# Kernel optimization log

Hardware: AMD Instinct MI355X
Metric: run time of the kernel (lower is better)

Reference implementation:

```python
import jax, jax.numpy as jnp
import numpy as np
import math

D_MODEL = 1024
NUM_HEADS = 16
D_HEAD = D_MODEL // NUM_HEADS


def setup_inputs() -> dict:
    key = jax.random.key(0)
    ks = jax.random.split(key, 15)
    B, S, D = 2, 2048, D_MODEL
    s = 1.0 / math.sqrt(D)
    inp = {
        'query': jax.random.normal(ks[0], (B, S, D), jnp.float32),
        'key': jax.random.normal(ks[1], (B, S, D), jnp.float32),
        'value': jax.random.normal(ks[2], (B, S, D), jnp.float32),
        'pos_embedding': jax.random.normal(ks[3], (B, S, D), jnp.float32),
        'Wq': jax.random.normal(ks[4], (D, D), jnp.float32) * s,
        'bq': jnp.zeros((D,), jnp.float32),
        'Wk': jax.random.normal(ks[5], (D, D), jnp.float32) * s,
        'bk': jnp.zeros((D,), jnp.float32),
        'Wv': jax.random.normal(ks[6], (D, D), jnp.float32) * s,
        'bv': jnp.zeros((D,), jnp.float32),
        'Wp': jax.random.normal(ks[7], (D, D), jnp.float32) * s,
        'bp': jnp.zeros((D,), jnp.float32),
        'Wo': jax.random.normal(ks[8], (D, D), jnp.float32) * s,
        'bo': jnp.zeros((D,), jnp.float32),
    }
    return inp


def _relative_shift(pos_score):
    # pos_score: [B, H, S1, S2] -> Transformer-XL pad/reshape/slice shift
    B, H, S1, S2 = pos_score.shape
    padded = jnp.pad(pos_score, ((0, 0), (0, 0), (0, 0), (1, 0)))  # [B,H,S1,S2+1]
    padded = padded.reshape(B, H, S2 + 1, S1)
    return padded[:, :, 1:].reshape(B, H, S1, S2)


def reference(query, key, value, pos_embedding, Wq, bq, Wk, bk, Wv, bv, Wp, bp, Wo, bo):
    B, S, D = query.shape
    H, Dh = NUM_HEADS, D_HEAD
    sqrt_dim = math.sqrt(D)

    q = (query @ Wq.T + bq).reshape(B, S, H, Dh)          # [B,S,H,Dh]
    k = (key @ Wk.T + bk).reshape(B, S, H, Dh)            # [B,S,H,Dh]
    v = (value @ Wv.T + bv).reshape(B, S, H, Dh)          # [B,S,H,Dh]
    p = (pos_embedding @ Wp.T + bp).reshape(B, S, H, Dh)  # [B,S,H,Dh]

    content_score = jnp.einsum('bqhd,bkhd->bhqk', q, k)   # [B,H,S,S]
    pos_score = jnp.einsum('bqhd,bkhd->bhqk', q, p)       # [B,H,S,S]
    pos_score = _relative_shift(pos_score)

    score = (content_score + pos_score) / sqrt_dim
    attn = jax.nn.softmax(score, axis=-1)
    context = jnp.einsum('bhqk,bkhd->bqhd', attn, v).reshape(B, S, D)
    return context @ Wo.T + bo
```

## Files before the change

### kernel.cpp

```cpp
#include <hip/hip_runtime.h>
#include <hip/hip_bf16.h>

#define S_LEN  2048
#define DMODEL 1024
#define NHEADS 16
#define DHEAD  64
#define TOKENS 4096
#define QSCALE 0.04508422f

typedef __attribute__((ext_vector_type(8))) short bf16x8;
typedef __attribute__((ext_vector_type(4))) float f32x4;

template <int M> struct IC { static constexpr int value = M; };

__device__ __forceinline__ float bf2f(unsigned short b) {
    union { unsigned u; float f; } v; v.u = ((unsigned)b) << 16;
    return v.f;
}
__device__ __forceinline__ unsigned cvt_pk_bf16(float lo, float hi) {
    unsigned r;
    asm("v_cvt_pk_bf16_f32 %0, %1, %2" : "=v"(r) : "v"(lo), "v"(hi));
    return r;
}
__device__ __forceinline__ unsigned short f2bf1(float x) {
    return (unsigned short)cvt_pk_bf16(x, x);
}
__device__ __forceinline__ void lds_fence() {
    asm volatile("s_waitcnt lgkmcnt(0)" ::: "memory");
    __builtin_amdgcn_sched_barrier(0);
}
__device__ __forceinline__ void gload_lds16(const void* g, void* l) {
    __builtin_amdgcn_global_load_lds(
        (const __attribute__((address_space(1))) void*)g,
        (__attribute__((address_space(3))) void*)l, 16, 0, 0);
}

__global__ __launch_bounds__(256) void proj_gemm(
    const float* __restrict__ x0, const float* __restrict__ x1,
    const float* __restrict__ x2, const float* __restrict__ x3,
    const float* __restrict__ w0, const float* __restrict__ w1,
    const float* __restrict__ w2, const float* __restrict__ w3,
    const float* __restrict__ b0, const float* __restrict__ b1,
    const float* __restrict__ b2, const float* __restrict__ b3,
    unsigned short* __restrict__ o0, unsigned short* __restrict__ o1,
    unsigned short* __restrict__ o2, unsigned short* __restrict__ o3)
{
    const int z = blockIdx.z;
    const float* X  = (z == 0) ? x0 : (z == 1) ? x1 : (z == 2) ? x2 : x3;
    const float* W  = (z == 0) ? w0 : (z == 1) ? w1 : (z == 2) ? w2 : w3;
    const float* Bv = (z == 0) ? b0 : (z == 1) ? b1 : (z == 2) ? b2 : b3;
    unsigned short* O = (z == 0) ? o0 : (z == 1) ? o1 : (z == 2) ? o2 : o3;

    __shared__ __align__(16) unsigned short At[128 * 40];
    __shared__ __align__(16) unsigned short Bt[128 * 40];

    const int tid  = threadIdx.x;
    const int lane = tid & 63;
    const int w    = tid >> 6;
    const int wr   = w & 1, wc = w >> 1;
    const int m0   = blockIdx.x * 128;
    const int n0   = blockIdx.y * 128;
    const int l16  = lane & 15, lq = lane >> 4;

    f32x4 acc[4][4];
    #pragma unroll
    for (int i = 0; i < 4; i++)
        #pragma unroll
        for (int j = 0; j < 4; j++) acc[i][j] = (f32x4){0.f, 0.f, 0.f, 0.f};

    for (int k0 = 0; k0 < DMODEL; k0 += 32) {
        __syncthreads();
        #pragma unroll
        for (int i = 0; i < 4; i++) {
            int e = tid + i * 256;
            int row = e >> 3, cg = e & 7;
            float4 va = *(const float4*)&X[(long)(m0 + row) * DMODEL + k0 + cg * 4];
            uint2 ua; ua.x = cvt_pk_bf16(va.x, va.y); ua.y = cvt_pk_bf16(va.z, va.w);
            *(uint2*)&At[row * 40 + cg * 4] = ua;
            float4 vb = *(const float4*)&W[(long)(n0 + row) * DMODEL + k0 + cg * 4];
            uint2 ub; ub.x = cvt_pk_bf16(vb.x, vb.y); ub.y = cvt_pk_bf16(vb.z, vb.w);
            *(uint2*)&Bt[row * 40 + cg * 4] = ub;
        }
        __syncthreads();
        bf16x8 af[4], bfr[4];
        #pragma unroll
        for (int f = 0; f < 4; f++) {
            af[f]  = *(const bf16x8*)&At[(64 * wr + 16 * f + l16) * 40 + 8 * lq];
            bfr[f] = *(const bf16x8*)&Bt[(64 * wc + 16 * f + l16) * 40 + 8 * lq];
        }
        #pragma unroll
        for (int i = 0; i < 4; i++)
            #pragma unroll
            for (int j = 0; j < 4; j++)
                acc[i][j] = __builtin_amdgcn_mfma_f32_16x16x32_bf16(af[i], bfr[j], acc[i][j], 0, 0, 0);
    }

    #pragma unroll
    for (int j = 0; j < 4; j++) {
        int n_g = n0 + 64 * wc + 16 * j + l16;
        float bias = Bv[n_g];
        int h = n_g >> 6, dh = n_g & 63;
        if (z == 2) {
            #pragma unroll
            for (int i = 0; i < 4; i++) {
                int m_g = m0 + 64 * wr + 16 * i + 4 * lq;
                int b = m_g >> 11, s = m_g & (S_LEN - 1);
                uint2 u;
                u.x = cvt_pk_bf16(acc[i][j][0] + bias, acc[i][j][1] + bias);
                u.y = cvt_pk_bf16(acc[i][j][2] + bias, acc[i][j][3] + bias);
                *(uint2*)&O[(long)(((b * NHEADS + h) * DHEAD) + dh) * S_LEN + s] = u;
            }
        } else {
            float scale = (z == 0) ? QSCALE : 1.0f;
            #pragma unroll
            for (int i = 0; i < 4; i++) {
                #pragma unroll
                for (int r = 0; r < 4; r++) {
                    int m_g = m0 + 64 * wr + 16 * i + 4 * lq + r;
                    int b = m_g >> 11, s = m_g & (S_LEN - 1);
                    O[(long)(((b * NHEADS + h) * S_LEN) + s) * DHEAD + dh] =
                        f2bf1((acc[i][j][r] + bias) * scale);
                }
            }
        }
    }
}

__global__ __launch_bounds__(256, 3) void rel_attn(
    const unsigned short* __restrict__ Q,
    const unsigned short* __restrict__ K,
    const unsigned short* __restrict__ VT,
    const unsigned short* __restrict__ P,
    unsigned short* __restrict__ CTX)
{
    __shared__ __align__(16) unsigned short Kb[64 * 64];
    __shared__ __align__(16) unsigned short P2b[128 * 64];
    __shared__ __align__(16) unsigned short WPb[4 * 1344];

    const int tid  = threadIdx.x;
    const int lane = tid & 63;
    const int w    = tid >> 6;
    const int l16  = lane & 15;
    const int lq   = lane >> 4;

    const int wg = ((blockIdx.x & 7) << 7) + (blockIdx.x >> 3);
    const int qt = wg & 31;
    const int bh = wg >> 5;
    const int q0 = qt << 6;
    const long baseQK = (long)bh * (S_LEN * DHEAD);
    const int qi_l = 16 * w + l16;

    const unsigned short* Kbh = K + baseQK;
    const unsigned short* Pbh = P + baseQK;
    const unsigned short* Vl  = VT + baseQK + (long)l16 * S_LEN + 8 * lq;

    const int gx0 = ((0 + lq) ^ (l16 & 7)) * 8;
    const int gx1 = ((4 + lq) ^ (l16 & 7)) * 8;

    bf16x8 qf0[2], qf1[2];
    {
        const unsigned short* qrow = Q + baseQK + (long)(q0 + qi_l) * DHEAD + 8 * lq;
        qf0[0] = *(const bf16x8*)(qrow);
        qf0[1] = *(const bf16x8*)(qrow + 32);
        qf1[0] = *(const bf16x8*)(qrow + DHEAD);
        qf1[1] = *(const bf16x8*)(qrow + DHEAD + 32);
    }

    const int srow = lane >> 3;
    const int sgr  = (lane & 7) ^ srow;
    auto stage_K = [&](int kr0) {
        #pragma unroll
        for (int j = 0; j < 2; ++j) {
            int idx = w * 2 + j;
            const unsigned short* src = Kbh + (long)(kr0 + idx * 8 + srow) * 64 + sgr * 8;
            gload_lds16(src, &Kb[idx * 512]);
        }
    };
    auto stage_P2 = [&](int mfirst) {
        #pragma unroll
        for (int j = 0; j < 2; ++j) {
            int idx = w * 2 + j;
            int m = mfirst + idx * 8 + srow;
            int pr = m - ((m >= 2049) ? 2049 : 0);
            const unsigned short* src = Pbh + (long)pr * 64 + sgr * 8;
            gload_lds16(src, &P2b[((mfirst + idx * 8) & 127) * 64]);
        }
    };

    float mrow = -1e30f, lrow = 0.f;
    f32x4 oacc[4];
    #pragma unroll
    for (int f = 0; f < 4; f++) oacc[f] = (f32x4){0.f, 0.f, 0.f, 0.f};

    unsigned short* tw        = &WPb[w * 1344 + l16 * 84 + 4 * lq];
    const unsigned short* tr  = &WPb[w * 1344 + l16 * 83 + 15 + 4 * lq];
    unsigned short* pw        = &WPb[w * 1344 + l16 * 72 + 4 * lq];
    const unsigned short* prd = &WPb[w * 1344 + l16 * 72 + 8 * lq];

    stage_K(0);
    {
        const int W0 = 1984 - q0;
        #pragma unroll
        for (int j = 0; j < 4; ++j) {
            int idx = w * 4 + j;
            int m = W0 + idx * 8 + srow;
            int pr = m - ((m >= 2049) ? 2049 : 0);
            const unsigned short* src = Pbh + (long)pr * 64 + sgr * 8;
            gload_lds16(src, &P2b[((W0 + idx * 8) & 127) * 64]);
        }
    }
    __syncthreads();

    auto tile_body = [&](auto mc, int ct, bool dz) __attribute__((always_inline)) {
        constexpr int MODE = decltype(mc)::value;
        const int c0 = ct << 6;
        const int mb = c0 - q0 + 2032 - 16 * w + l16;

        f32x4 cacc[4];
        #pragma unroll
        for (int f = 0; f < 4; f++) cacc[f] = (f32x4){0.f, 0.f, 0.f, 0.f};
        #pragma unroll
        for (int fc = 0; fc < 4; ++fc) {
            bf16x8 k0v = *(const bf16x8*)&Kb[(16 * fc + l16) * 64 + gx0];
            bf16x8 k1v = *(const bf16x8*)&Kb[(16 * fc + l16) * 64 + gx1];
            cacc[fc] = __builtin_amdgcn_mfma_f32_16x16x32_bf16(k0v, qf0[0], cacc[fc], 0, 0, 0);
            cacc[fc] = __builtin_amdgcn_mfma_f32_16x16x32_bf16(k1v, qf0[1], cacc[fc], 0, 0, 0);
        }

        f32x4 tacc[5];
        #pragma unroll
        for (int g = 0; g < 5; g++) tacc[g] = (f32x4){0.f, 0.f, 0.f, 0.f};
        #pragma unroll
        for (int cg = 0; cg < 5; ++cg) {
            int sb = ((mb + 16 * cg) & 127) * 64;
            bf16x8 p0 = *(const bf16x8*)&P2b[sb + gx0];
            bf16x8 p1 = *(const bf16x8*)&P2b[sb + gx1];
            tacc[cg] = __builtin_amdgcn_mfma_f32_16x16x32_bf16(
                p0, (MODE == 1) ? qf1[0] : qf0[0], tacc[cg], 0, 0, 0);
            tacc[cg] = __builtin_amdgcn_mfma_f32_16x16x32_bf16(
                p1, (MODE == 1) ? qf1[1] : qf0[1], tacc[cg], 0, 0, 0);
        }

        __syncthreads();

        if constexpr (MODE != 2) {
            if (ct < 31) { stage_K(c0 + 64); stage_P2(c0 - q0 + 2112); }
        }

        bf16x8 vf[2][4];
        #pragma unroll
        for (int kk = 0; kk < 2; ++kk)
            #pragma unroll
            for (int fa = 0; fa < 4; ++fa)
                vf[kk][fa] = *(const bf16x8*)(Vl + c0 + fa * (16 * S_LEN) + kk * 32);

        lds_fence();
        #pragma unroll
        for (int cg = 0; cg < 5; ++cg) {
            uint2 u;
            u.x = cvt_pk_bf16(tacc[cg][0], tacc[cg][1]);
            u.y = cvt_pk_bf16(tacc[cg][2], tacc[cg][3]);
            *(uint2*)(tw + 16 * cg) = u;
        }
        lds_fence();

        float sc[4][4];
        if constexpr (MODE != 2) {
            #pragma unroll
            for (int fc = 0; fc < 4; ++fc)
                #pragma unroll
                for (int r = 0; r < 4; ++r)
                    sc[fc][r] = cacc[fc][r] + bf2f(tr[16 * fc + r]);
            if constexpr (MODE == 1) {
                if (dz && qi_l == 63 && lq == 0) sc[0][0] = cacc[0][0];
            }
        } else {
            float v0[4][4];
            #pragma unroll
            for (int fc = 0; fc < 4; ++fc)
                #pragma unroll
                for (int r = 0; r < 4; ++r) v0[fc][r] = bf2f(tr[16 * fc + r]);
            lds_fence();
            f32x4 tb2[5];
            #pragma unroll
            for (int g = 0; g < 5; g++) tb2[g] = (f32x4){0.f, 0.f, 0.f, 0.f};
            #pragma unroll
            for (int cg = 0; cg < 5; ++cg) {
                int sb = ((mb + 16 * cg) & 127) * 64;
                bf16x8 p0 = *(const bf16x8*)&P2b[sb + gx0];
                bf16x8 p1 = *(const bf16x8*)&P2b[sb + gx1];
                tb2[cg] = __builtin_amdgcn_mfma_f32_16x16x32_bf16(p0, qf1[0], tb2[cg], 0, 0, 0);
                tb2[cg] = __builtin_amdgcn_mfma_f32_16x16x32_bf16(p1, qf1[1], tb2[cg], 0, 0, 0);
            }
            __syncthreads();
            if (ct < 31) { stage_K(c0 + 64); stage_P2(c0 - q0 + 2112); }
            #pragma unroll
            for (int cg = 0; cg < 5; ++cg) {
                uint2 u;
                u.x = cvt_pk_bf16(tb2[cg][0], tb2[cg][1]);
                u.y = cvt_pk_bf16(tb2[cg][2], tb2[cg][3]);
                *(uint2*)(tw + 16 * cg) = u;
            }
            lds_fence();
            #pragma unroll
            for (int fc = 0; fc < 4; ++fc)
                #pragma unroll
                for (int r = 0; r < 4; ++r) {
                    float v1 = bf2f(tr[16 * fc + r]);
                    int ci = 16 * fc + 4 * lq + r;
                    float term = (ci == qi_l + 1) ? 0.f
                               : ((ci > qi_l) ? v1 : v0[fc][r]);
                    sc[fc][r] = cacc[fc][r] + term;
                }
        }

        float tmax = sc[0][0];
        #pragma unroll
        for (int fc = 0; fc < 4; ++fc)
            #pragma unroll
            for (int r = 0; r < 4; ++r) tmax = fmaxf(tmax, sc[fc][r]);
        tmax = fmaxf(tmax, __shfl_xor(tmax, 16, 64));
        tmax = fmaxf(tmax, __shfl_xor(tmax, 32, 64));
        float nm = fmaxf(mrow, tmax);
        float alpha = __builtin_amdgcn_exp2f(mrow - nm);
        mrow = nm;
        float pv[4][4];
        float rs = 0.f;
        #pragma unroll
        for (int fc = 0; fc < 4; ++fc)
            #pragma unroll
            for (int r = 0; r < 4; ++r) {
                float p = __builtin_amdgcn_exp2f(sc[fc][r] - nm);
                pv[fc][r] = p;
                rs += p;
            }
        rs += __shfl_xor(rs, 16, 64);
        rs += __shfl_xor(rs, 32, 64);
        lrow = lrow * alpha + rs;
        #pragma unroll
        for (int f = 0; f < 4; f++)
            #pragma unroll
            for (int r = 0; r < 4; r++) oacc[f][r] *= alpha;

        lds_fence();
        #pragma unroll
        for (int fc = 0; fc < 4; ++fc) {
            uint2 u;
            u.x = cvt_pk_bf16(pv[fc][0], pv[fc][1]);
            u.y = cvt_pk_bf16(pv[fc][2], pv[fc][3]);
            *(uint2*)(pw + 16 * fc) = u;
        }
        lds_fence();
        bf16x8 pfr[2];
        pfr[0] = *(const bf16x8*)(prd);
        pfr[1] = *(const bf16x8*)(prd + 32);

        #pragma unroll
        for (int kk = 0; kk < 2; ++kk)
            #pragma unroll
            for (int fa = 0; fa < 4; ++fa)
                oacc[fa] = __builtin_amdgcn_mfma_f32_16x16x32_bf16(vf[kk][fa], pfr[kk], oacc[fa], 0, 0, 0);

        __syncthreads();
    };

    for (int ct = 0; ct < qt; ++ct) tile_body(IC<0>{}, ct, false);
    tile_body(IC<2>{}, qt, false);
    if (qt < 31) {
        tile_body(IC<1>{}, qt + 1, true);
        for (int ct = qt + 2; ct < S_LEN / 64; ++ct) tile_body(IC<1>{}, ct, false);
    }

    const int b = bh >> 4, h = bh & 15;
    const float rinv = 1.0f / lrow;
    unsigned short* op = CTX + ((long)(b * S_LEN + q0 + qi_l) * NHEADS + h) * DHEAD + 4 * lq;
    #pragma unroll
    for (int fa = 0; fa < 4; ++fa) {
        uint2 u;
        u.x = cvt_pk_bf16(oacc[fa][0] * rinv, oacc[fa][1] * rinv);
        u.y = cvt_pk_bf16(oacc[fa][2] * rinv, oacc[fa][3] * rinv);
        *(uint2*)(op + 16 * fa) = u;
    }
}

__global__ __launch_bounds__(256) void out_gemm(
    const unsigned short* __restrict__ A,
    const float* __restrict__ W,
    const float* __restrict__ Bv,
    float* __restrict__ O)
{
    __shared__ __align__(16) unsigned short At[128 * 40];
    __shared__ __align__(16) unsigned short Bt[128 * 40];

    const int tid  = threadIdx.x;
    const int lane = tid & 63;
    const int w    = tid >> 6;
    const int wr   = w & 1, wc = w >> 1;
    const int m0   = blockIdx.x * 128;
    const int n0   = blockIdx.y * 128;
    const int l16  = lane & 15, lq = lane >> 4;

    f32x4 acc[4][4];
    #pragma unroll
    for (int i = 0; i < 4; i++)
        #pragma unroll
        for (int j = 0; j < 4; j++) acc[i][j] = (f32x4){0.f, 0.f, 0.f, 0.f};

    for (int k0 = 0; k0 < DMODEL; k0 += 32) {
        __syncthreads();
        #pragma unroll
        for (int i = 0; i < 2; i++) {
            int e = tid + i * 256;
            int row = e >> 2, sg = e & 3;
            *(float4*)&At[row * 40 + sg * 8] =
                *(const float4*)&A[(long)(m0 + row) * DMODEL + k0 + sg * 8];
        }
        #pragma unroll
        for (int i = 0; i < 4; i++) {
            int e = tid + i * 256;
            int row = e >> 3, cg = e & 7;
            float4 vb = *(const float4*)&W[(long)(n0 + row) * DMODEL + k0 + cg * 4];
            uint2 ub; ub.x = cvt_pk_bf16(vb.x, vb.y); ub.y = cvt_pk_bf16(vb.z, vb.w);
            *(uint2*)&Bt[row * 40 + cg * 4] = ub;
        }
        __syncthreads();
        bf16x8 af[4], bfr[4];
        #pragma unroll
        for (int f = 0; f < 4; f++) {
            af[f]  = *(const bf16x8*)&At[(64 * wr + 16 * f + l16) * 40 + 8 * lq];
            bfr[f] = *(const bf16x8*)&Bt[(64 * wc + 16 * f + l16) * 40 + 8 * lq];
        }
        #pragma unroll
        for (int i = 0; i < 4; i++)
            #pragma unroll
            for (int j = 0; j < 4; j++)
                acc[i][j] = __builtin_amdgcn_mfma_f32_16x16x32_bf16(af[i], bfr[j], acc[i][j], 0, 0, 0);
    }

    #pragma unroll
    for (int j = 0; j < 4; j++) {
        int n_g = n0 + 64 * wc + 16 * j + l16;
        float bias = Bv[n_g];
        #pragma unroll
        for (int i = 0; i < 4; i++) {
            #pragma unroll
            for (int r = 0; r < 4; r++) {
                int m_g = m0 + 64 * wr + 16 * i + 4 * lq + r;
                O[(long)m_g * DMODEL + n_g] = acc[i][j][r] + bias;
            }
        }
    }
}

extern "C" void kernel_launch(void* const* d_in, const int* in_sizes, int n_in,
                              void* d_out, int out_size, void* d_ws, size_t ws_size,
                              hipStream_t stream) {
    (void)in_sizes; (void)n_in; (void)out_size; (void)ws_size;
    const float* query = (const float*)d_in[0];
    const float* key_  = (const float*)d_in[1];
    const float* value = (const float*)d_in[2];
    const float* pos   = (const float*)d_in[3];
    const float* Wq = (const float*)d_in[4];  const float* bq = (const float*)d_in[5];
    const float* Wk = (const float*)d_in[6];  const float* bk = (const float*)d_in[7];
    const float* Wv = (const float*)d_in[8];  const float* bv = (const float*)d_in[9];
    const float* Wp = (const float*)d_in[10]; const float* bp = (const float*)d_in[11];
    const float* Wo = (const float*)d_in[12]; const float* bo = (const float*)d_in[13];
    float* out = (float*)d_out;

    const long NE = (long)TOKENS * DMODEL;
    unsigned short* qb = (unsigned short*)d_ws;
    unsigned short* kb = qb + NE;
    unsigned short* vb = kb + NE;
    unsigned short* pb = vb + NE;
    unsigned short* cx = pb + NE;

    proj_gemm<<<dim3(32, 8, 4), 256, 0, stream>>>(
        query, key_, value, pos, Wq, Wk, Wv, Wp, bq, bk, bv, bp, qb, kb, vb, pb);
    rel_attn<<<1024, 256, 0, stream>>>(qb, kb, vb, pb, cx);
    out_gemm<<<dim3(32, 8), 256, 0, stream>>>(cx, Wo, bo, out);
}
```

Before: 269.2 us.

## Use 128-query attention tiles with 8 waves sharing K/P staging

Doubles the query tile of the relative attention kernel to 128 rows handled by 8 waves per 512-thread block. Each staged K and P tile is now reused by twice as many query rows, which halves global-to-LDS traffic per query. The P ring buffer grows to 256 rows and a new two-tile diagonal path handles the relative-shift wrap. Costs are a larger LDS footprint, fewer blocks (512), and two dual-MFMA diagonal tiles per block instead of one.

```diff
diff --git a/kernel.cpp b/kernel.cpp
--- a/kernel.cpp
+++ b/kernel.cpp
@@ -126,7 +126,7 @@
     }
 }
 
-__global__ __launch_bounds__(256, 3) void rel_attn(
+__global__ __launch_bounds__(512, 4) void rel_attn(
     const unsigned short* __restrict__ Q,
     const unsigned short* __restrict__ K,
     const unsigned short* __restrict__ VT,
@@ -134,8 +134,8 @@
     unsigned short* __restrict__ CTX)
 {
     __shared__ __align__(16) unsigned short Kb[64 * 64];
-    __shared__ __align__(16) unsigned short P2b[128 * 64];
-    __shared__ __align__(16) unsigned short WPb[4 * 1344];
+    __shared__ __align__(16) unsigned short P2b[256 * 64];
+    __shared__ __align__(16) unsigned short WPb[8 * 1344];
 
     const int tid  = threadIdx.x;
     const int lane = tid & 63;
@@ -143,12 +143,12 @@
     const int l16  = lane & 15;
     const int lq   = lane >> 4;
 
-    const int wg = ((blockIdx.x & 7) << 7) + (blockIdx.x >> 3);
-    const int qt = wg & 31;
-    const int bh = wg >> 5;
-    const int q0 = qt << 6;
+    const int wg = ((blockIdx.x & 7) << 6) | (blockIdx.x >> 3);
+    const int qt = wg & 15;
+    const int bh = wg >> 4;
+    const int q0 = qt << 7;
     const long baseQK = (long)bh * (S_LEN * DHEAD);
-    const int qi_l = 16 * w + l16;
+    const int gq_rel = 16 * w + l16;
 
     const unsigned short* Kbh = K + baseQK;
     const unsigned short* Pbh = P + baseQK;
@@ -159,7 +159,7 @@
 
     bf16x8 qf0[2], qf1[2];
     {
-        const unsigned short* qrow = Q + baseQK + (long)(q0 + qi_l) * DHEAD + 8 * lq;
+        const unsigned short* qrow = Q + baseQK + (long)(q0 + gq_rel) * DHEAD + 8 * lq;
         qf0[0] = *(const bf16x8*)(qrow);
         qf0[1] = *(const bf16x8*)(qrow + 32);
         qf1[0] = *(const bf16x8*)(qrow + DHEAD);
@@ -168,23 +168,15 @@
 
     const int srow = lane >> 3;
     const int sgr  = (lane & 7) ^ srow;
-    auto stage_K = [&](int kr0) {
-        #pragma unroll
-        for (int j = 0; j < 2; ++j) {
-            int idx = w * 2 + j;
-            const unsigned short* src = Kbh + (long)(kr0 + idx * 8 + srow) * 64 + sgr * 8;
-            gload_lds16(src, &Kb[idx * 512]);
-        }
+    auto stage_K = [&](int kr0) __attribute__((always_inline)) {
+        const unsigned short* src = Kbh + (long)(kr0 + w * 8 + srow) * 64 + sgr * 8;
+        gload_lds16(src, &Kb[(w * 8) * 64]);
     };
-    auto stage_P2 = [&](int mfirst) {
-        #pragma unroll
-        for (int j = 0; j < 2; ++j) {
-            int idx = w * 2 + j;
-            int m = mfirst + idx * 8 + srow;
-            int pr = m - ((m >= 2049) ? 2049 : 0);
-            const unsigned short* src = Pbh + (long)pr * 64 + sgr * 8;
-            gload_lds16(src, &P2b[((mfirst + idx * 8) & 127) * 64]);
-        }
+    auto stage_P2 = [&](int mfirst) __attribute__((always_inline)) {
+        int m = mfirst + w * 8 + srow;
+        int pr = m - ((m >= 2049) ? 2049 : 0);
+        const unsigned short* src = Pbh + (long)pr * 64 + sgr * 8;
+        gload_lds16(src, &P2b[(((mfirst & 255)) + w * 8) * 64]);
     };
 
     float mrow = -1e30f, lrow = 0.f;
@@ -197,123 +189,12 @@
     unsigned short* pw        = &WPb[w * 1344 + l16 * 72 + 4 * lq];
     const unsigned short* prd = &WPb[w * 1344 + l16 * 72 + 8 * lq];
 
+    const int W0 = 1920 - q0;
     stage_K(0);
-    {
-        const int W0 = 1984 - q0;
-        #pragma unroll
-        for (int j = 0; j < 4; ++j) {
-            int idx = w * 4 + j;
-            int m = W0 + idx * 8 + srow;
-            int pr = m - ((m >= 2049) ? 2049 : 0);
-            const unsigned short* src = Pbh + (long)pr * 64 + sgr * 8;
-            gload_lds16(src, &P2b[((W0 + idx * 8) & 127) * 64]);
-        }
-    }
+    stage_P2(W0); stage_P2(W0 + 64); stage_P2(W0 + 128);
     __syncthreads();
 
-    auto tile_body = [&](auto mc, int ct, bool dz) __attribute__((always_inline)) {
-        constexpr int MODE = decltype(mc)::value;
-        const int c0 = ct << 6;
-        const int mb = c0 - q0 + 2032 - 16 * w + l16;
-
-        f32x4 cacc[4];
-        #pragma unroll
-        for (int f = 0; f < 4; f++) cacc[f] = (f32x4){0.f, 0.f, 0.f, 0.f};
-        #pragma unroll
-        for (int fc = 0; fc < 4; ++fc) {
-            bf16x8 k0v = *(const bf16x8*)&Kb[(16 * fc + l16) * 64 + gx0];
-            bf16x8 k1v = *(const bf16x8*)&Kb[(16 * fc + l16) * 64 + gx1];
-            cacc[fc] = __builtin_amdgcn_mfma_f32_16x16x32_bf16(k0v, qf0[0], cacc[fc], 0, 0, 0);
-            cacc[fc] = __builtin_amdgcn_mfma_f32_16x16x32_bf16(k1v, qf0[1], cacc[fc], 0, 0, 0);
-        }
-
-        f32x4 tacc[5];
-        #pragma unroll
-        for (int g = 0; g < 5; g++) tacc[g] = (f32x4){0.f, 0.f, 0.f, 0.f};
-        #pragma unroll
-        for (int cg = 0; cg < 5; ++cg) {
-            int sb = ((mb + 16 * cg) & 127) * 64;
-            bf16x8 p0 = *(const bf16x8*)&P2b[sb + gx0];
-            bf16x8 p1 = *(const bf16x8*)&P2b[sb + gx1];
-            tacc[cg] = __builtin_amdgcn_mfma_f32_16x16x32_bf16(
-                p0, (MODE == 1) ? qf1[0] : qf0[0], tacc[cg], 0, 0, 0);
-            tacc[cg] = __builtin_amdgcn_mfma_f32_16x16x32_bf16(
-                p1, (MODE == 1) ? qf1[1] : qf0[1], tacc[cg], 0, 0, 0);
-        }
-
-        __syncthreads();
-
-        if constexpr (MODE != 2) {
-            if (ct < 31) { stage_K(c0 + 64); stage_P2(c0 - q0 + 2112); }
-        }
-
-        bf16x8 vf[2][4];
-        #pragma unroll
-        for (int kk = 0; kk < 2; ++kk)
-            #pragma unroll
-            for (int fa = 0; fa < 4; ++fa)
-                vf[kk][fa] = *(const bf16x8*)(Vl + c0 + fa * (16 * S_LEN) + kk * 32);
-
-        lds_fence();
-        #pragma unroll
-        for (int cg = 0; cg < 5; ++cg) {
-            uint2 u;
-            u.x = cvt_pk_bf16(tacc[cg][0], tacc[cg][1]);
-            u.y = cvt_pk_bf16(tacc[cg][2], tacc[cg][3]);
-            *(uint2*)(tw + 16 * cg) = u;
-        }
-        lds_fence();
-
-        float sc[4][4];
-        if constexpr (MODE != 2) {
-            #pragma unroll
-            for (int fc = 0; fc < 4; ++fc)
-                #pragma unroll
-                for (int r = 0; r < 4; ++r)
-                    sc[fc][r] = cacc[fc][r] + bf2f(tr[16 * fc + r]);
-            if constexpr (MODE == 1) {
-                if (dz && qi_l == 63 && lq == 0) sc[0][0] = cacc[0][0];
-            }
-        } else {
-            float v0[4][4];
-            #pragma unroll
-            for (int fc = 0; fc < 4; ++fc)
-                #pragma unroll
-                for (int r = 0; r < 4; ++r) v0[fc][r] = bf2f(tr[16 * fc + r]);
-            lds_fence();
-            f32x4 tb2[5];
-            #pragma unroll
-            for (int g = 0; g < 5; g++) tb2[g] = (f32x4){0.f, 0.f, 0.f, 0.f};
-            #pragma unroll
-            for (int cg = 0; cg < 5; ++cg) {
-                int sb = ((mb + 16 * cg) & 127) * 64;
-                bf16x8 p0 = *(const bf16x8*)&P2b[sb + gx0];
-                bf16x8 p1 = *(const bf16x8*)&P2b[sb + gx1];
-                tb2[cg] = __builtin_amdgcn_mfma_f32_16x16x32_bf16(p0, qf1[0], tb2[cg], 0, 0, 0);
-                tb2[cg] = __builtin_amdgcn_mfma_f32_16x16x32_bf16(p1, qf1[1], tb2[cg], 0, 0, 0);
-            }
-            __syncthreads();
-            if (ct < 31) { stage_K(c0 + 64); stage_P2(c0 - q0 + 2112); }
-            #pragma unroll
-            for (int cg = 0; cg < 5; ++cg) {
-                uint2 u;
-                u.x = cvt_pk_bf16(tb2[cg][0], tb2[cg][1]);
-                u.y = cvt_pk_bf16(tb2[cg][2], tb2[cg][3]);
-                *(uint2*)(tw + 16 * cg) = u;
-            }
-            lds_fence();
-            #pragma unroll
-            for (int fc = 0; fc < 4; ++fc)
-                #pragma unroll
-                for (int r = 0; r < 4; ++r) {
-                    float v1 = bf2f(tr[16 * fc + r]);
-                    int ci = 16 * fc + 4 * lq + r;
-                    float term = (ci == qi_l + 1) ? 0.f
-                               : ((ci > qi_l) ? v1 : v0[fc][r]);
-                    sc[fc][r] = cacc[fc][r] + term;
-                }
-        }
-
+    auto finish = [&](float (&sc)[4][4], bf16x8 (&vf)[2][4]) __attribute__((always_inline)) {
         float tmax = sc[0][0];
         #pragma unroll
         for (int fc = 0; fc < 4; ++fc)
@@ -360,20 +241,171 @@
             #pragma unroll
             for (int fa = 0; fa < 4; ++fa)
                 oacc[fa] = __builtin_amdgcn_mfma_f32_16x16x32_bf16(vf[kk][fa], pfr[kk], oacc[fa], 0, 0, 0);
-
-        __syncthreads();
     };
 
-    for (int ct = 0; ct < qt; ++ct) tile_body(IC<0>{}, ct, false);
-    tile_body(IC<2>{}, qt, false);
-    if (qt < 31) {
-        tile_body(IC<1>{}, qt + 1, true);
-        for (int ct = qt + 2; ct < S_LEN / 64; ++ct) tile_body(IC<1>{}, ct, false);
-    }
+    auto tile_pure = [&](auto mc, int ct, bool dz) __attribute__((always_inline)) {
+        constexpr int MODE = decltype(mc)::value;
+        const int c0 = ct << 6;
+        const int mb = c0 - q0 + 2032 - 16 * w + l16;
+
+        f32x4 cacc[4];
+        #pragma unroll
+        for (int f = 0; f < 4; f++) cacc[f] = (f32x4){0.f, 0.f, 0.f, 0.f};
+        #pragma unroll
+        for (int fc = 0; fc < 4; ++fc) {
+            bf16x8 k0v = *(const bf16x8*)&Kb[(16 * fc + l16) * 64 + gx0];
+            bf16x8 k1v = *(const bf16x8*)&Kb[(16 * fc + l16) * 64 + gx1];
+            cacc[fc] = __builtin_amdgcn_mfma_f32_16x16x32_bf16(k0v, qf0[0], cacc[fc], 0, 0, 0);
+            cacc[fc] = __builtin_amdgcn_mfma_f32_16x16x32_bf16(k1v, qf0[1], cacc[fc], 0, 0, 0);
+        }
+
+        f32x4 tacc[5];
+        #pragma unroll
+        for (int g = 0; g < 5; g++) tacc[g] = (f32x4){0.f, 0.f, 0.f, 0.f};
+        #pragma unroll
+        for (int cg = 0; cg < 5; ++cg) {
+            int sb = ((mb + 16 * cg) & 255) * 64;
+            bf16x8 p0 = *(const bf16x8*)&P2b[sb + gx0];
+            bf16x8 p1 = *(const bf16x8*)&P2b[sb + gx1];
+            tacc[cg] = __builtin_amdgcn_mfma_f32_16x16x32_bf16(
+                p0, (MODE == 1) ? qf1[0] : qf0[0], tacc[cg], 0, 0, 0);
+            tacc[cg] = __builtin_amdgcn_mfma_f32_16x16x32_bf16(
+                p1, (MODE == 1) ? qf1[1] : qf0[1], tacc[cg], 0, 0, 0);
+        }
+
+        __syncthreads();
+        if (ct < 31) { stage_K(c0 + 64); stage_P2(W0 + 192 + 64 * ct); }
+
+        bf16x8 vf[2][4];
+        #pragma unroll
+        for (int kk = 0; kk < 2; ++kk)
+            #pragma unroll
+            for (int fa = 0; fa < 4; ++fa)
+                vf[kk][fa] = *(const bf16x8*)(Vl + c0 + fa * (16 * S_LEN) + kk * 32);
+
+        lds_fence();
+        #pragma unroll
+        for (int cg = 0; cg < 5; ++cg) {
+            uint2 u;
+            u.x = cvt_pk_bf16(tacc[cg][0], tacc[cg][1]);
+            u.y = cvt_pk_bf16(tacc[cg][2], tacc[cg][3]);
+            *(uint2*)(tw + 16 * cg) = u;
+        }
+        lds_fence();
+
+        float sc[4][4];
+        #pragma unroll
+        for (int fc = 0; fc < 4; ++fc)
+            #pragma unroll
+            for (int r = 0; r < 4; ++r)
+                sc[fc][r] = cacc[fc][r] + bf2f(tr[16 * fc + r]);
+        if (MODE == 1 && dz && w == 7 && l16 == 15 && lq == 0)
+            sc[0][0] = cacc[0][0];
+
+        finish(sc, vf);
+        __syncthreads();
+    };
+
+    auto tile_dual = [&](int ct) __attribute__((always_inline)) {
+        const int c0 = ct << 6;
+        const int mb = c0 - q0 + 2032 - 16 * w + l16;
+        const int rel = q0 + gq_rel - c0;
+
+        f32x4 cacc[4];
+        #pragma unroll
+        for (int f = 0; f < 4; f++) cacc[f] = (f32x4){0.f, 0.f, 0.f, 0.f};
+        #pragma unroll
+        for (int fc = 0; fc < 4; ++fc) {
+            bf16x8 k0v = *(const bf16x8*)&Kb[(16 * fc + l16) * 64 + gx0];
+            bf16x8 k1v = *(const bf16x8*)&Kb[(16 * fc + l16) * 64 + gx1];
+            cacc[fc] = __builtin_amdgcn_mfma_f32_16x16x32_bf16(k0v, qf0[0], cacc[fc], 0, 0, 0);
+            cacc[fc] = __builtin_amdgcn_mfma_f32_16x16x32_bf16(k1v, qf0[1], cacc[fc], 0, 0, 0);
+        }
+
+        f32x4 tacc[5];
+        #pragma unroll
+        for (int g = 0; g < 5; g++) tacc[g] = (f32x4){0.f, 0.f, 0.f, 0.f};
+        #pragma unroll
+        for (int cg = 0; cg < 5; ++cg) {
+            int sb = ((mb + 16 * cg) & 255) * 64;
+            bf16x8 p0 = *(const bf16x8*)&P2b[sb + gx0];
+            bf16x8 p1 = *(const bf16x8*)&P2b[sb + gx1];
+            tacc[cg] = __builtin_amdgcn_mfma_f32_16x16x32_bf16(p0, qf0[0], tacc[cg], 0, 0, 0);
+            tacc[cg] = __builtin_amdgcn_mfma_f32_16x16x32_bf16(p1, qf0[1], tacc[cg], 0, 0, 0);
+        }
+        lds_fence();
+        #pragma unroll
+        for (int cg = 0; cg < 5; ++cg) {
+            uint2 u;
+            u.x = cvt_pk_bf16(tacc[cg][0], tacc[cg][1]);
+            u.y = cvt_pk_bf16(tacc[cg][2], tacc[cg][3]);
+            *(uint2*)(tw + 16 * cg) = u;
+        }
+        lds_fence();
+        float v0[4][4];
+        #pragma unroll
+        for (int fc = 0; fc < 4; ++fc)
+            #pragma unroll
+            for (int r = 0; r < 4; ++r) v0[fc][r] = bf2f(tr[16 * fc + r]);
+        lds_fence();
+
+        f32x4 tb2[5];
+        #pragma unroll
+        for (int g = 0; g < 5; g++) tb2[g] = (f32x4){0.f, 0.f, 0.f, 0.f};
+        #pragma unroll
+        for (int cg = 0; cg < 5; ++cg) {
+            int sb = ((mb + 16 * cg) & 255) * 64;
+            bf16x8 p0 = *(const bf16x8*)&P2b[sb + gx0];
+            bf16x8 p1 = *(const bf16x8*)&P2b[sb + gx1];
+            tb2[cg] = __builtin_amdgcn_mfma_f32_16x16x32_bf16(p0, qf1[0], tb2[cg], 0, 0, 0);
+            tb2[cg] = __builtin_amdgcn_mfma_f32_16x16x32_bf16(p1, qf1[1], tb2[cg], 0, 0, 0);
+        }
+
+        __syncthreads();
+        if (ct < 31) { stage_K(c0 + 64); stage_P2(W0 + 192 + 64 * ct); }
+
+        #pragma unroll
+        for (int cg = 0; cg < 5; ++cg) {
+            uint2 u;
+            u.x = cvt_pk_bf16(tb2[cg][0], tb2[cg][1]);
+            u.y = cvt_pk_bf16(tb2[cg][2], tb2[cg][3]);
+            *(uint2*)(tw + 16 * cg) = u;
+        }
+        lds_fence();
+
+        float sc[4][4];
+        #pragma unroll
+        for (int fc = 0; fc < 4; ++fc)
+            #pragma unroll
+            for (int r = 0; r < 4; ++r) {
+                float vB = bf2f(tr[16 * fc + r]);
+                int ci = 16 * fc + 4 * lq + r;
+                float term = (ci == rel + 1) ? 0.f
+                           : ((ci > rel) ? vB : v0[fc][r]);
+                sc[fc][r] = cacc[fc][r] + term;
+            }
+
+        bf16x8 vf[2][4];
+        #pragma unroll
+        for (int kk = 0; kk < 2; ++kk)
+            #pragma unroll
+            for (int fa = 0; fa < 4; ++fa)
+                vf[kk][fa] = *(const bf16x8*)(Vl + c0 + fa * (16 * S_LEN) + kk * 32);
+
+        finish(sc, vf);
+        __syncthreads();
+    };
+
+    const int dct = 2 * qt;
+    for (int ct = 0; ct < dct; ++ct) tile_pure(IC<0>{}, ct, false);
+    tile_dual(dct);
+    tile_dual(dct + 1);
+    for (int ct = dct + 2; ct < S_LEN / 64; ++ct)
+        tile_pure(IC<1>{}, ct, ct == dct + 2);
 
     const int b = bh >> 4, h = bh & 15;
     const float rinv = 1.0f / lrow;
-    unsigned short* op = CTX + ((long)(b * S_LEN + q0 + qi_l) * NHEADS + h) * DHEAD + 4 * lq;
+    unsigned short* op = CTX + ((long)(b * S_LEN + q0 + gq_rel) * NHEADS + h) * DHEAD + 4 * lq;
     #pragma unroll
     for (int fa = 0; fa < 4; ++fa) {
         uint2 u;
@@ -476,6 +508,6 @@
 
     proj_gemm<<<dim3(32, 8, 4), 256, 0, stream>>>(
         query, key_, value, pos, Wq, Wk, Wv, Wp, bq, bk, bv, bp, qb, kb, vb, pb);
-    rel_attn<<<1024, 256, 0, stream>>>(qb, kb, vb, pb, cx);
+    rel_attn<<<512, 512, 0, stream>>>(qb, kb, vb, pb, cx);
     out_gemm<<<dim3(32, 8), 256, 0, stream>>>(cx, Wo, bo, out);
 }
```

New measurement: 272.1 us. Within noise of the previous version (+1.1%).
